# Performance work log

Measured on AMD Instinct MI355X. Metric: run time of the kernel, lower is better.

Reference implementation:

```python
import jax, jax.numpy as jnp
import numpy as np

EPS = 1e-3  # tf.keras.layers.BatchNormalization default epsilon


def setup_inputs() -> dict:
    key = jax.random.key(0)
    k1, k2 = jax.random.split(key)
    B, N, F = 16, 8192, 256
    voxel_features = jax.random.normal(k1, (B, N, F), dtype=jnp.float32)
    num_valid_voxels = jax.random.randint(k2, (B,), 0, N, dtype=jnp.int32)
    gamma = jnp.ones((F,), dtype=jnp.float32)
    beta = jnp.zeros((F,), dtype=jnp.float32)
    return {
        "voxel_features": voxel_features,
        "num_valid_voxels": num_valid_voxels,
        "gamma": gamma,
        "beta": beta,
    }


def reference(voxel_features, num_valid_voxels, gamma, beta):
    # voxel_features: [B, N, F]; num_valid_voxels: [B]
    B, N, F = voxel_features.shape
    # mask[b, n] = n < num_valid_voxels[b]
    mask = (jnp.arange(N, dtype=jnp.int32)[None, :] < num_valid_voxels[:, None])
    maskf = mask.astype(voxel_features.dtype)[:, :, None]  # [B, N, 1]
    count = jnp.maximum(jnp.sum(num_valid_voxels).astype(voxel_features.dtype), 1.0)
    xm = voxel_features * maskf
    # Batch statistics over valid voxels only (per-feature), biased variance as BN uses
    mean = jnp.sum(xm, axis=(0, 1)) / count                      # [F]
    var = jnp.sum((voxel_features - mean) ** 2 * maskf, axis=(0, 1)) / count  # [F]
    inv_std = jax.lax.rsqrt(var + EPS)
    normed = (voxel_features - mean) * inv_std * gamma + beta
    # Padding positions are zeroed (the original pads unpadded outputs with zeros)
    return normed * maskf
```

## Files before the change

### kernel.cpp

```cpp
#include <hip/hip_runtime.h>

#define Bdim 16
#define Ndim 8192
#define Fdim 256
#define EPS 1e-3f

#define RED_BLOCKS_PER_BATCH 64
#define RED_BLOCKS (Bdim * RED_BLOCKS_PER_BATCH)
#define RED_ROWS_PER_BLOCK (Ndim / RED_BLOCKS_PER_BATCH)

#define NORM_BLOCKS 8192
#define TOTAL_CHUNKS (Bdim * Ndim * (Fdim / 4))

typedef float fx4 __attribute__((ext_vector_type(4)));


__global__ __launch_bounds__(512) void init_kernel(float* __restrict__ ws) {
    ws[threadIdx.x] = 0.0f;
}

__global__ __launch_bounds__(256) void reduce_kernel(
    const float* __restrict__ x, const int* __restrict__ nv,
    float* __restrict__ ws)
{
    __shared__ float lds_s[4][Fdim];
    __shared__ float lds_q[4][Fdim];
    const int tid = threadIdx.x;
    const int b   = blockIdx.x >> 6;
    const int rb0 = (blockIdx.x & 63) * RED_ROWS_PER_BLOCK;
    const int nvb = nv[b];
    int valid = nvb - rb0;
    valid = valid < 0 ? 0 : (valid > RED_ROWS_PER_BLOCK ? RED_ROWS_PER_BLOCK : valid);

    const int c = tid & 63;
    const int r = tid >> 6;
    const fx4* xb = (const fx4*)(x + ((size_t)b * Ndim + rb0) * Fdim) + c;

    float s0=0.f,s1=0.f,s2=0.f,s3=0.f, q0=0.f,q1=0.f,q2=0.f,q3=0.f;

    int i = r;
    for (; i + 12 < valid; i += 16) {
        const fx4 v0 = xb[(size_t)(i     ) * 64];
        const fx4 v1 = xb[(size_t)(i +  4) * 64];
        const fx4 v2 = xb[(size_t)(i +  8) * 64];
        const fx4 v3 = xb[(size_t)(i + 12) * 64];
        s0 += v0.x; q0 += v0.x*v0.x;  s1 += v0.y; q1 += v0.y*v0.y;
        s2 += v0.z; q2 += v0.z*v0.z;  s3 += v0.w; q3 += v0.w*v0.w;
        s0 += v1.x; q0 += v1.x*v1.x;  s1 += v1.y; q1 += v1.y*v1.y;
        s2 += v1.z; q2 += v1.z*v1.z;  s3 += v1.w; q3 += v1.w*v1.w;
        s0 += v2.x; q0 += v2.x*v2.x;  s1 += v2.y; q1 += v2.y*v2.y;
        s2 += v2.z; q2 += v2.z*v2.z;  s3 += v2.w; q3 += v2.w*v2.w;
        s0 += v3.x; q0 += v3.x*v3.x;  s1 += v3.y; q1 += v3.y*v3.y;
        s2 += v3.z; q2 += v3.z*v3.z;  s3 += v3.w; q3 += v3.w*v3.w;
    }
    for (; i < valid; i += 4) {
        const fx4 v = xb[(size_t)i * 64];
        s0 += v.x; q0 += v.x*v.x;  s1 += v.y; q1 += v.y*v.y;
        s2 += v.z; q2 += v.z*v.z;  s3 += v.w; q3 += v.w*v.w;
    }

    const int f0 = c * 4;
    lds_s[r][f0+0]=s0; lds_s[r][f0+1]=s1; lds_s[r][f0+2]=s2; lds_s[r][f0+3]=s3;
    lds_q[r][f0+0]=q0; lds_q[r][f0+1]=q1; lds_q[r][f0+2]=q2; lds_q[r][f0+3]=q3;
    __syncthreads();

    float ts = 0.0f, tq = 0.0f;
    #pragma unroll
    for (int rr = 0; rr < 4; rr++) { ts += lds_s[rr][tid]; tq += lds_q[rr][tid]; }
    unsafeAtomicAdd(&ws[tid], ts);
    unsafeAtomicAdd(&ws[Fdim + tid], tq);
}

__global__ __launch_bounds__(256) void norm_kernel(
    const float* __restrict__ x, const int* __restrict__ nv,
    const float* __restrict__ gamma, const float* __restrict__ beta,
    const float* __restrict__ ws, float* __restrict__ out)
{
    __shared__ float s_sc[Fdim], s_bi[Fdim];
    __shared__ int s_nv[Bdim];
    const int tid = threadIdx.x;
    if (tid < Bdim) s_nv[tid] = nv[tid];
    __syncthreads();
    {
        int cnt = 0;
        #pragma unroll
        for (int i = 0; i < Bdim; i++) cnt += s_nv[i];
        const float inv_count = 1.0f / fmaxf((float)cnt, 1.0f);
        const float mean = ws[tid] * inv_count;
        float var = fmaf(ws[Fdim + tid], inv_count, -mean * mean);
        var = fmaxf(var, 0.0f);
        const float s = rsqrtf(var + EPS) * gamma[tid];
        s_sc[tid] = s;
        s_bi[tid] = fmaf(-mean, s, beta[tid]);
    }
    __syncthreads();

    const int c = tid & 63;
    const fx4 sc = ((const fx4*)s_sc)[c];
    const fx4 bi = ((const fx4*)s_bi)[c];

    const int base = blockIdx.x * 256 + tid;
    const int stride = NORM_BLOCKS * 256;
    #pragma unroll
    for (int it = 0; it < TOTAL_CHUNKS / (NORM_BLOCKS * 256); it++) {
        const int idx = base + it * stride;
        const int row = idx >> 6;
        const int b = row >> 13;
        const int n = row & (Ndim - 1);
        fx4* po = (fx4*)out + idx;
        if (n < s_nv[b]) {
            const fx4 v = ((const fx4*)x)[idx];
            fx4 o;
            o.x = fmaf(v.x, sc.x, bi.x);
            o.y = fmaf(v.y, sc.y, bi.y);
            o.z = fmaf(v.z, sc.z, bi.z);
            o.w = fmaf(v.w, sc.w, bi.w);
            __builtin_nontemporal_store(o, po);
        } else {
            const fx4 z = {0.f, 0.f, 0.f, 0.f};
            __builtin_nontemporal_store(z, po);
        }
    }
}

extern "C" void kernel_launch(void* const* d_in, const int* in_sizes, int n_in,
                              void* d_out, int out_size, void* d_ws, size_t ws_size,
                              hipStream_t stream) {
    const float* x     = (const float*)d_in[0];
    const int*   nv    = (const int*)d_in[1];
    const float* gamma = (const float*)d_in[2];
    const float* beta  = (const float*)d_in[3];
    float* out = (float*)d_out;
    float* ws  = (float*)d_ws;

    init_kernel<<<1, 512, 0, stream>>>(ws);
    reduce_kernel<<<RED_BLOCKS, 256, 0, stream>>>(x, nv, ws);
    norm_kernel<<<NORM_BLOCKS, 256, 0, stream>>>(x, nv, gamma, beta, ws, out);
}
```

Baseline: 235.0 us.

## Balance reduction work across blocks by prefix-summed valid rows

```diff
diff --git a/kernel.cpp b/kernel.cpp
--- a/kernel.cpp
+++ b/kernel.cpp
@@ -5,12 +5,10 @@
 #define Fdim 256
 #define EPS 1e-3f
 
-#define RED_BLOCKS_PER_BATCH 64
-#define RED_BLOCKS (Bdim * RED_BLOCKS_PER_BATCH)
-#define RED_ROWS_PER_BLOCK (Ndim / RED_BLOCKS_PER_BATCH)
-
-#define NORM_BLOCKS 8192
+#define RED_BLOCKS 512
+#define NORM_BLOCKS 2048
 #define TOTAL_CHUNKS (Bdim * Ndim * (Fdim / 4))
+#define NORM_ITERS (TOTAL_CHUNKS / (NORM_BLOCKS * 256))
 
 typedef float fx4 __attribute__((ext_vector_type(4)));
 
@@ -25,25 +23,47 @@
 {
     __shared__ float lds_s[4][Fdim];
     __shared__ float lds_q[4][Fdim];
+    __shared__ int s_pre[Bdim + 1];
     const int tid = threadIdx.x;
-    const int b   = blockIdx.x >> 6;
-    const int rb0 = (blockIdx.x & 63) * RED_ROWS_PER_BLOCK;
-    const int nvb = nv[b];
-    int valid = nvb - rb0;
-    valid = valid < 0 ? 0 : (valid > RED_ROWS_PER_BLOCK ? RED_ROWS_PER_BLOCK : valid);
+    if (tid == 0) {
+        int acc = 0;
+        s_pre[0] = 0;
+        #pragma unroll
+        for (int i = 0; i < Bdim; i++) { acc += nv[i]; s_pre[i + 1] = acc; }
+    }
+    __syncthreads();
+
+    const int V = s_pre[Bdim];
+    const int per = V / RED_BLOCKS, rem = V % RED_BLOCKS;
+    const int g = blockIdx.x;
+    const int k0 = g * per + (g < rem ? g : rem);
+    const int kE = k0 + per + (g < rem ? 1 : 0);
 
     const int c = tid & 63;
     const int r = tid >> 6;
-    const fx4* xb = (const fx4*)(x + ((size_t)b * Ndim + rb0) * Fdim) + c;
+    const fx4* xc = (const fx4*)x + c;
 
     float s0=0.f,s1=0.f,s2=0.f,s3=0.f, q0=0.f,q1=0.f,q2=0.f,q3=0.f;
 
-    int i = r;
-    for (; i + 12 < valid; i += 16) {
-        const fx4 v0 = xb[(size_t)(i     ) * 64];
-        const fx4 v1 = xb[(size_t)(i +  4) * 64];
-        const fx4 v2 = xb[(size_t)(i +  8) * 64];
-        const fx4 v3 = xb[(size_t)(i + 12) * 64];
+    int k = k0 + r;
+    int b = 0, pre_b = 0, pre_next = s_pre[1];
+    if (k < kE) {
+        while (k >= pre_next) { ++b; pre_b = pre_next; pre_next = s_pre[b + 1]; }
+    }
+
+    #define ROW_OF(kk, rowvar)                                                  \
+        while ((kk) >= pre_next) { ++b; pre_b = pre_next; pre_next = s_pre[b+1]; } \
+        const int rowvar = (b << 13) + ((kk) - pre_b);
+
+    for (; k + 12 < kE; k += 16) {
+        ROW_OF(k,      row0)
+        ROW_OF(k + 4,  row1)
+        ROW_OF(k + 8,  row2)
+        ROW_OF(k + 12, row3)
+        const fx4 v0 = xc[(size_t)row0 * 64];
+        const fx4 v1 = xc[(size_t)row1 * 64];
+        const fx4 v2 = xc[(size_t)row2 * 64];
+        const fx4 v3 = xc[(size_t)row3 * 64];
         s0 += v0.x; q0 += v0.x*v0.x;  s1 += v0.y; q1 += v0.y*v0.y;
         s2 += v0.z; q2 += v0.z*v0.z;  s3 += v0.w; q3 += v0.w*v0.w;
         s0 += v1.x; q0 += v1.x*v1.x;  s1 += v1.y; q1 += v1.y*v1.y;
@@ -53,11 +73,13 @@
         s0 += v3.x; q0 += v3.x*v3.x;  s1 += v3.y; q1 += v3.y*v3.y;
         s2 += v3.z; q2 += v3.z*v3.z;  s3 += v3.w; q3 += v3.w*v3.w;
     }
-    for (; i < valid; i += 4) {
-        const fx4 v = xb[(size_t)i * 64];
+    for (; k < kE; k += 4) {
+        ROW_OF(k, row)
+        const fx4 v = xc[(size_t)row * 64];
         s0 += v.x; q0 += v.x*v.x;  s1 += v.y; q1 += v.y*v.y;
         s2 += v.z; q2 += v.z*v.z;  s3 += v.w; q3 += v.w*v.w;
     }
+    #undef ROW_OF
 
     const int f0 = c * 4;
     lds_s[r][f0+0]=s0; lds_s[r][f0+1]=s1; lds_s[r][f0+2]=s2; lds_s[r][f0+3]=s3;
@@ -102,7 +124,7 @@
     const int base = blockIdx.x * 256 + tid;
     const int stride = NORM_BLOCKS * 256;
     #pragma unroll
-    for (int it = 0; it < TOTAL_CHUNKS / (NORM_BLOCKS * 256); it++) {
+    for (int it = 0; it < NORM_ITERS; it++) {
         const int idx = base + it * stride;
         const int row = idx >> 6;
         const int b = row >> 13;
```

After: 236.6 us. No clear change (+0.7%).
